# Performance work log

Measured on AMD Instinct MI355X. Metric: run time of the kernel, lower is better.

The kernel has to match this reference:

```python
import jax, jax.numpy as jnp
import numpy as np

N = 8
A_NUM = 5
ALPHA = [0.01, 0.25, 0.5, 0.9, 0.99]
EPS = 1e-10
BATCH = 262144


def _cayley(bias, n):
    # Build lower-triangular matrix exactly as torch code: row i+1 gets bias[i:2*i+1]
    b = bias.reshape(-1)
    L = jnp.zeros((n, n), dtype=bias.dtype)
    for i in range(n - 1):  # tiny fixed loop (n=8)
        L = L.at[i + 1, : i + 1].set(b[i : 2 * i + 1])
    Bm = L - L.T  # antisymmetric
    I = jnp.eye(n, dtype=bias.dtype)
    # MatrixExp = inv(I - Bm) @ (I + Bm)  (Cayley transform)
    return jnp.linalg.solve(I - Bm, I + Bm)


def _translate(A, bias, n):
    Q = _cayley(bias, n)
    # Q @ A @ Q^T, batched over leading dim
    return jnp.einsum('ij,bjk,lk->bil', Q, A, Q)


def _nus(M, W, eps):
    # weighted sum over the a_num axis with normalized squared weights
    w = W[:, 0] ** 2
    w = w / (w.sum() + eps)
    return jnp.einsum('a,banm->bnm', w, M)


def setup_inputs() -> dict:
    key = jax.random.key(0)
    ks = jax.random.split(key, 9)
    n2 = N * N
    return {
        'x': jax.random.normal(ks[0], (BATCH, n2), dtype=jnp.float32),
        'states': jax.random.normal(ks[1], (BATCH, A_NUM * n2), dtype=jnp.float32),
        'kernel_r': jax.random.uniform(ks[2], (A_NUM, 1), dtype=jnp.float32),
        'kernel_t': jax.random.uniform(ks[3], (1, 1), dtype=jnp.float32),
        'kernel_phi': jax.random.uniform(ks[4], (1, 1), dtype=jnp.float32),
        'kernel_s': jax.random.uniform(ks[5], (A_NUM, 1), dtype=jnp.float32),
        'bias_r': jax.random.uniform(ks[6], (N * (N - 1) // 2, 1), dtype=jnp.float32),
        'bias_t': jax.random.uniform(ks[7], (N * (N - 1) // 2, 1), dtype=jnp.float32),
        'bias_y': jax.random.uniform(ks[8], (N * (N - 1) // 2, 1), dtype=jnp.float32),
    }


def reference(x, states, kernel_r, kernel_t, kernel_phi, kernel_s, bias_r, bias_t, bias_y):
    n, a_num, eps = N, A_NUM, EPS
    Xt = x.reshape(-1, n, n)
    Mt_1 = states.reshape(-1, a_num, n, n)

    Yt = _nus(Mt_1, kernel_r, eps)              # [B,n,n]
    Rt = _translate(Yt, bias_r, n)

    t = kernel_t ** 2 / (kernel_t ** 2 + kernel_phi ** 2 + eps)  # (1,1) scalar gate
    Tt = (1.0 - t) * Xt + t * Rt                # FM
    Phit = _translate(Tt, bias_t, n)

    alpha = jnp.asarray(ALPHA, dtype=x.dtype)[None, :, None, None]
    Mt = (1.0 - alpha) * Mt_1 + alpha * Phit[:, None, :, :]      # [B,a,n,n]

    St = _nus(Mt, kernel_s, eps)
    Ot = _translate(St, bias_y, n)

    output = Ot.reshape(-1, n * n)
    out_state = Mt.reshape(-1, a_num * n * n)
    return output, out_state
```

## Files before the change

### kernel.cpp

```cpp
#include <hip/hip_runtime.h>

#define ANUM 5
#define EPS 1e-10f

__global__ void precompute_kernel(const float* __restrict__ kernel_r,
                                  const float* __restrict__ kernel_t,
                                  const float* __restrict__ kernel_phi,
                                  const float* __restrict__ kernel_s,
                                  const float* __restrict__ bias_r,
                                  const float* __restrict__ bias_t,
                                  const float* __restrict__ bias_y,
                                  float* __restrict__ ws) {
  __shared__ float sQ[3][64];
  const int tid = threadIdx.x;
  if (tid < 3) {
    const float* bias = (tid == 0) ? bias_r : (tid == 1) ? bias_t : bias_y;

    float Bm[8][8];
#pragma unroll
    for (int a = 0; a < 8; ++a)
#pragma unroll
      for (int b = 0; b < 8; ++b) Bm[a][b] = 0.f;
#pragma unroll
    for (int a = 0; a < 7; ++a) {
#pragma unroll 8
      for (int c = 0; c < 7; ++c) {
        if (c <= a) {
          float v = bias[a + c];
          Bm[a + 1][c] = v;
          Bm[c][a + 1] = -v;
        }
      }
    }
    float A[8][8], C[8][8];
#pragma unroll
    for (int a = 0; a < 8; ++a)
#pragma unroll
      for (int b = 0; b < 8; ++b) {
        float id = (a == b) ? 1.f : 0.f;
        A[a][b] = id - Bm[a][b];
        C[a][b] = id + Bm[a][b];
      }
#pragma unroll
    for (int p = 0; p < 8; ++p) {
      float inv = 1.f / A[p][p];
#pragma unroll
      for (int b = 0; b < 8; ++b) { A[p][b] *= inv; C[p][b] *= inv; }
#pragma unroll
      for (int r = 0; r < 8; ++r) {
        if (r == p) continue;
        float f = A[r][p];
#pragma unroll
        for (int b = 0; b < 8; ++b) { A[r][b] -= f * A[p][b]; C[r][b] -= f * C[p][b]; }
      }
    }
#pragma unroll
    for (int a = 0; a < 8; ++a)
#pragma unroll
      for (int b = 0; b < 8; ++b) sQ[tid][a * 8 + b] = C[a][b];
  } else if (tid == 3) {
    float sr = 0.f, ss = 0.f;
#pragma unroll
    for (int a = 0; a < ANUM; ++a) sr += kernel_r[a] * kernel_r[a];
#pragma unroll
    for (int a = 0; a < ANUM; ++a) ws[192 + a] = kernel_r[a] * kernel_r[a] / (sr + EPS);
#pragma unroll
    for (int a = 0; a < ANUM; ++a) ss += kernel_s[a] * kernel_s[a];
#pragma unroll
    for (int a = 0; a < ANUM; ++a) ws[197 + a] = kernel_s[a] * kernel_s[a] / (ss + EPS);
    float kt2 = kernel_t[0] * kernel_t[0];
    float kp2 = kernel_phi[0] * kernel_phi[0];
    ws[202] = kt2 / (kt2 + kp2 + EPS);
  }
  __syncthreads();
  const int i = tid >> 3, j = tid & 7;
  float acc = 0.f;
#pragma unroll
  for (int k = 0; k < 8; ++k) acc += sQ[1][i * 8 + k] * sQ[0][k * 8 + j];
  ws[tid]       = sQ[1][tid];
  ws[64 + tid]  = acc;
  ws[128 + tid] = sQ[2][tid];
}

__device__ __forceinline__ float dot8(float4 a0, float4 a1, float4 b0, float4 b1) {
  return a0.x * b0.x + a0.y * b0.y + a0.z * b0.z + a0.w * b0.w +
         a1.x * b1.x + a1.y * b1.y + a1.z * b1.z + a1.w * b1.w;
}

#define LGKM0() asm volatile("s_waitcnt lgkmcnt(0)" ::: "memory")

__launch_bounds__(256, 4)
__global__ void spdsru_kernel(const float* __restrict__ x,
                              const float* __restrict__ states,
                              const float* __restrict__ ws,
                              float* __restrict__ out,
                              float* __restrict__ out_state,
                              int B, int ITER, int W) {
  __shared__ __align__(16) float lds[4][4][64];
  const int tid = threadIdx.x;
  const int lane = tid & 63;
  const int wv = tid >> 6;
  const int i = lane >> 3, j = lane & 7;
  float* b0 = lds[wv][0];
  float* b1 = lds[wv][1];
  float* b2 = lds[wv][2];
  float* b3 = lds[wv][3];

  const float4 Qti0 = *(const float4*)(ws + 0 + i * 8);
  const float4 Qti1 = *(const float4*)(ws + 0 + i * 8 + 4);
  const float4 Qtj0 = *(const float4*)(ws + 0 + j * 8);
  const float4 Qtj1 = *(const float4*)(ws + 0 + j * 8 + 4);
  const float4 Q1i0 = *(const float4*)(ws + 64 + i * 8);
  const float4 Q1i1 = *(const float4*)(ws + 64 + i * 8 + 4);
  const float4 Q1j0 = *(const float4*)(ws + 64 + j * 8);
  const float4 Q1j1 = *(const float4*)(ws + 64 + j * 8 + 4);
  const float4 Qyi0 = *(const float4*)(ws + 128 + i * 8);
  const float4 Qyi1 = *(const float4*)(ws + 128 + i * 8 + 4);
  const float4 Qyj0 = *(const float4*)(ws + 128 + j * 8);
  const float4 Qyj1 = *(const float4*)(ws + 128 + j * 8 + 4);
  const float wr0 = ws[192], wr1 = ws[193], wr2 = ws[194], wr3 = ws[195], wr4 = ws[196];
  const float ks0 = ws[197], ks1 = ws[198], ks2 = ws[199], ks3 = ws[200], ks4 = ws[201];
  const float tg = ws[202];

  const int wave = (blockIdx.x * 256 + tid) >> 6;

  int b = wave;
  float X = 0.f, M0 = 0.f, M1 = 0.f, M2 = 0.f, M3 = 0.f, M4 = 0.f;
  if (b < B) {
    const float* S = states + (size_t)b * 320;
    X  = x[(size_t)b * 64 + lane];
    M0 = S[0 * 64 + lane];
    M1 = S[1 * 64 + lane];
    M2 = S[2 * 64 + lane];
    M3 = S[3 * 64 + lane];
    M4 = S[4 * 64 + lane];
  }

  for (int it = 0; it < ITER; ++it) {
    const int bn = b + W;
    float Xn = 0.f, N0 = 0.f, N1 = 0.f, N2 = 0.f, N3 = 0.f, N4 = 0.f;
    if (it + 1 < ITER && bn < B) {
      const float* Sn = states + (size_t)bn * 320;
      Xn = x[(size_t)bn * 64 + lane];
      N0 = Sn[0 * 64 + lane];
      N1 = Sn[1 * 64 + lane];
      N2 = Sn[2 * 64 + lane];
      N3 = Sn[3 * 64 + lane];
      N4 = Sn[4 * 64 + lane];
    }

    const float Yt = wr0 * M0 + wr1 * M1 + wr2 * M2 + wr3 * M3 + wr4 * M4;

    b0[lane] = X;
    b2[lane] = Yt;
    LGKM0();
    {
      float4 xr0 = *(const float4*)(b0 + i * 8);
      float4 xr1 = *(const float4*)(b0 + i * 8 + 4);
      float4 yr0 = *(const float4*)(b2 + i * 8);
      float4 yr1 = *(const float4*)(b2 + i * 8 + 4);
      float vx = dot8(xr0, xr1, Qtj0, Qtj1);
      float vy = dot8(yr0, yr1, Q1j0, Q1j1);
      b1[j * 8 + i] = vx;
      b3[j * 8 + i] = vy;
    }
    LGKM0();
    float XT, YT;
    {
      float4 xc0 = *(const float4*)(b1 + j * 8);
      float4 xc1 = *(const float4*)(b1 + j * 8 + 4);
      float4 yc0 = *(const float4*)(b3 + j * 8);
      float4 yc1 = *(const float4*)(b3 + j * 8 + 4);
      XT = dot8(xc0, xc1, Qti0, Qti1);
      YT = dot8(yc0, yc1, Q1i0, Q1i1);
    }
    const float Ph = (1.f - tg) * XT + tg * YT;

    M0 = (1.0f - 0.01f) * M0 + 0.01f * Ph;
    M1 = (1.0f - 0.25f) * M1 + 0.25f * Ph;
    M2 = (1.0f - 0.5f)  * M2 + 0.5f  * Ph;
    M3 = (1.0f - 0.9f)  * M3 + 0.9f  * Ph;
    M4 = (1.0f - 0.99f) * M4 + 0.99f * Ph;

    if (b < B) {
      float* SO = out_state + (size_t)b * 320;
      SO[0 * 64 + lane] = M0;
      SO[1 * 64 + lane] = M1;
      SO[2 * 64 + lane] = M2;
      SO[3 * 64 + lane] = M3;
      SO[4 * 64 + lane] = M4;
    }

    const float St = ks0 * M0 + ks1 * M1 + ks2 * M2 + ks3 * M3 + ks4 * M4;
    b0[lane] = St;
    LGKM0();
    {
      float4 r0 = *(const float4*)(b0 + i * 8);
      float4 r1 = *(const float4*)(b0 + i * 8 + 4);
      float v = dot8(r0, r1, Qyj0, Qyj1);
      b1[j * 8 + i] = v;
    }
    LGKM0();
    float Ot;
    {
      float4 c0 = *(const float4*)(b1 + j * 8);
      float4 c1 = *(const float4*)(b1 + j * 8 + 4);
      Ot = dot8(c0, c1, Qyi0, Qyi1);
    }
    if (b < B) out[(size_t)b * 64 + lane] = Ot;

    X = Xn; M0 = N0; M1 = N1; M2 = N2; M3 = N3; M4 = N4;
    b = bn;
  }
}

extern "C" void kernel_launch(void* const* d_in, const int* in_sizes, int n_in,
                              void* d_out, int out_size, void* d_ws, size_t ws_size,
                              hipStream_t stream) {
  const float* x          = (const float*)d_in[0];
  const float* states     = (const float*)d_in[1];
  const float* kernel_r   = (const float*)d_in[2];
  const float* kernel_t   = (const float*)d_in[3];
  const float* kernel_phi = (const float*)d_in[4];
  const float* kernel_s   = (const float*)d_in[5];
  const float* bias_r     = (const float*)d_in[6];
  const float* bias_t     = (const float*)d_in[7];
  const float* bias_y     = (const float*)d_in[8];
  float* ws = (float*)d_ws;
  float* out = (float*)d_out;

  const int B = in_sizes[0] / 64;
  float* out_state = out + (size_t)B * 64;

  precompute_kernel<<<1, 64, 0, stream>>>(kernel_r, kernel_t, kernel_phi, kernel_s,
                                          bias_r, bias_t, bias_y, ws);

  const int blocks = 2048;
  const int W = blocks * 4;
  const int ITER = (B + W - 1) / W;
  spdsru_kernel<<<blocks, 256, 0, stream>>>(x, states, ws, out, out_state, B, ITER, W);
}
```

Measured before the change: 665.3 us.

## Fold output translate into one LDS round via precomposed Cayley products

Expands St algebraically into a mix of the old states, X and Y. The output rotation is then computed in the same two LDS transpose rounds as the Phi path, using precomposed matrices Qy*Qt and Qy*Qt*Qr scaled by square-root gate factors. This removes the serial dependency on the state update and two extra LDS round trips per matrix. In exchange each lane does more dot products and holds more matrix registers. The launch bound drops its minimum occupancy hint, and sqrt-based scaling may shift rounding slightly.

```diff
diff --git a/kernel.cpp b/kernel.cpp
--- a/kernel.cpp
+++ b/kernel.cpp
@@ -11,7 +11,7 @@
                                   const float* __restrict__ bias_t,
                                   const float* __restrict__ bias_y,
                                   float* __restrict__ ws) {
-  __shared__ float sQ[3][64];
+  __shared__ float sQ[4][64];
   const int tid = threadIdx.x;
   if (tid < 3) {
     const float* bias = (tid == 0) ? bias_r : (tid == 1) ? bias_t : bias_y;
@@ -58,28 +58,48 @@
     for (int a = 0; a < 8; ++a)
 #pragma unroll
       for (int b = 0; b < 8; ++b) sQ[tid][a * 8 + b] = C[a][b];
-  } else if (tid == 3) {
-    float sr = 0.f, ss = 0.f;
-#pragma unroll
-    for (int a = 0; a < ANUM; ++a) sr += kernel_r[a] * kernel_r[a];
-#pragma unroll
-    for (int a = 0; a < ANUM; ++a) ws[192 + a] = kernel_r[a] * kernel_r[a] / (sr + EPS);
-#pragma unroll
-    for (int a = 0; a < ANUM; ++a) ss += kernel_s[a] * kernel_s[a];
-#pragma unroll
-    for (int a = 0; a < ANUM; ++a) ws[197 + a] = kernel_s[a] * kernel_s[a] / (ss + EPS);
-    float kt2 = kernel_t[0] * kernel_t[0];
-    float kp2 = kernel_phi[0] * kernel_phi[0];
-    ws[202] = kt2 / (kt2 + kp2 + EPS);
   }
   __syncthreads();
   const int i = tid >> 3, j = tid & 7;
-  float acc = 0.f;
-#pragma unroll
-  for (int k = 0; k < 8; ++k) acc += sQ[1][i * 8 + k] * sQ[0][k * 8 + j];
-  ws[tid]       = sQ[1][tid];
-  ws[64 + tid]  = acc;
-  ws[128 + tid] = sQ[2][tid];
+  float q1 = 0.f;
+#pragma unroll
+  for (int k = 0; k < 8; ++k) q1 += sQ[1][i * 8 + k] * sQ[0][k * 8 + j];
+  sQ[3][tid] = q1;
+  __syncthreads();
+  float q2 = 0.f, q3 = 0.f;
+#pragma unroll
+  for (int k = 0; k < 8; ++k) {
+    q2 += sQ[2][i * 8 + k] * sQ[1][k * 8 + j];
+    q3 += sQ[2][i * 8 + k] * sQ[3][k * 8 + j];
+  }
+  float sr = 0.f, ss = 0.f;
+#pragma unroll
+  for (int a = 0; a < ANUM; ++a) sr += kernel_r[a] * kernel_r[a];
+#pragma unroll
+  for (int a = 0; a < ANUM; ++a) ss += kernel_s[a] * kernel_s[a];
+  const float alpha[ANUM] = {0.01f, 0.25f, 0.5f, 0.9f, 0.99f};
+  float c = 0.f;
+#pragma unroll
+  for (int a = 0; a < ANUM; ++a)
+    c += (kernel_s[a] * kernel_s[a] / (ss + EPS)) * alpha[a];
+  float kt2 = kernel_t[0] * kernel_t[0];
+  float kp2 = kernel_phi[0] * kernel_phi[0];
+  float t = kt2 / (kt2 + kp2 + EPS);
+
+  const float s1 = sqrtf(1.f - t);
+  const float s2 = sqrtf(t);
+  const float s3 = sqrtf(c * (1.f - t));
+  const float s4 = sqrtf(c * t);
+
+  ws[tid]        = sQ[1][tid] * s1;
+  ws[64 + tid]   = sQ[3][tid] * s2;
+  ws[128 + tid]  = sQ[2][tid];
+  ws[192 + tid]  = q2 * s3;
+  ws[256 + tid]  = q3 * s4;
+  if (tid < ANUM) {
+    ws[320 + tid] = kernel_r[tid] * kernel_r[tid] / (sr + EPS);
+    ws[325 + tid] = (kernel_s[tid] * kernel_s[tid] / (ss + EPS)) * (1.f - alpha[tid]);
+  }
 }
 
 __device__ __forceinline__ float dot8(float4 a0, float4 a1, float4 b0, float4 b1) {
@@ -88,39 +108,41 @@
 }
 
 #define LGKM0() asm volatile("s_waitcnt lgkmcnt(0)" ::: "memory")
-
-__launch_bounds__(256, 4)
+#define UNI(nm, idx) \
+  const float nm = __int_as_float(__builtin_amdgcn_readfirstlane(__float_as_int(ws[idx])));
+
+__launch_bounds__(256)
 __global__ void spdsru_kernel(const float* __restrict__ x,
                               const float* __restrict__ states,
                               const float* __restrict__ ws,
                               float* __restrict__ out,
                               float* __restrict__ out_state,
                               int B, int ITER, int W) {
-  __shared__ __align__(16) float lds[4][4][64];
+  __shared__ __align__(16) float lds[4][5][64];
   const int tid = threadIdx.x;
   const int lane = tid & 63;
   const int wv = tid >> 6;
   const int i = lane >> 3, j = lane & 7;
-  float* b0 = lds[wv][0];
-  float* b1 = lds[wv][1];
-  float* b2 = lds[wv][2];
+  float* bX = lds[wv][0];
+  float* bY = lds[wv][1];
+  float* bS = lds[wv][2];
   float* b3 = lds[wv][3];
-
-  const float4 Qti0 = *(const float4*)(ws + 0 + i * 8);
-  const float4 Qti1 = *(const float4*)(ws + 0 + i * 8 + 4);
-  const float4 Qtj0 = *(const float4*)(ws + 0 + j * 8);
-  const float4 Qtj1 = *(const float4*)(ws + 0 + j * 8 + 4);
-  const float4 Q1i0 = *(const float4*)(ws + 64 + i * 8);
-  const float4 Q1i1 = *(const float4*)(ws + 64 + i * 8 + 4);
-  const float4 Q1j0 = *(const float4*)(ws + 64 + j * 8);
-  const float4 Q1j1 = *(const float4*)(ws + 64 + j * 8 + 4);
-  const float4 Qyi0 = *(const float4*)(ws + 128 + i * 8);
-  const float4 Qyi1 = *(const float4*)(ws + 128 + i * 8 + 4);
-  const float4 Qyj0 = *(const float4*)(ws + 128 + j * 8);
-  const float4 Qyj1 = *(const float4*)(ws + 128 + j * 8 + 4);
-  const float wr0 = ws[192], wr1 = ws[193], wr2 = ws[194], wr3 = ws[195], wr4 = ws[196];
-  const float ks0 = ws[197], ks1 = ws[198], ks2 = ws[199], ks3 = ws[200], ks4 = ws[201];
-  const float tg = ws[202];
+  float* b4 = lds[wv][4];
+
+#define LOADQ(nm, off)                                          \
+  const float4 nm##i0 = *(const float4*)(ws + off + i * 8);     \
+  const float4 nm##i1 = *(const float4*)(ws + off + i * 8 + 4); \
+  const float4 nm##j0 = *(const float4*)(ws + off + j * 8);     \
+  const float4 nm##j1 = *(const float4*)(ws + off + j * 8 + 4);
+  LOADQ(Qt, 0)
+  LOADQ(Q1, 64)
+  LOADQ(Qy, 128)
+  LOADQ(Q2, 192)
+  LOADQ(Q3, 256)
+#undef LOADQ
+
+  UNI(wr0, 320) UNI(wr1, 321) UNI(wr2, 322) UNI(wr3, 323) UNI(wr4, 324)
+  UNI(w20, 325) UNI(w21, 326) UNI(w22, 327) UNI(w23, 328) UNI(w24, 329)
 
   const int wave = (blockIdx.x * 256 + tid) >> 6;
 
@@ -150,32 +172,51 @@
     }
 
     const float Yt = wr0 * M0 + wr1 * M1 + wr2 * M2 + wr3 * M3 + wr4 * M4;
-
-    b0[lane] = X;
-    b2[lane] = Yt;
+    const float S0 = w20 * M0 + w21 * M1 + w22 * M2 + w23 * M3 + w24 * M4;
+
+    bX[lane] = X;
+    bY[lane] = Yt;
+    bS[lane] = S0;
     LGKM0();
     {
-      float4 xr0 = *(const float4*)(b0 + i * 8);
-      float4 xr1 = *(const float4*)(b0 + i * 8 + 4);
-      float4 yr0 = *(const float4*)(b2 + i * 8);
-      float4 yr1 = *(const float4*)(b2 + i * 8 + 4);
-      float vx = dot8(xr0, xr1, Qtj0, Qtj1);
-      float vy = dot8(yr0, yr1, Q1j0, Q1j1);
-      b1[j * 8 + i] = vx;
-      b3[j * 8 + i] = vy;
+      float4 xr0 = *(const float4*)(bX + i * 8);
+      float4 xr1 = *(const float4*)(bX + i * 8 + 4);
+      float4 yr0 = *(const float4*)(bY + i * 8);
+      float4 yr1 = *(const float4*)(bY + i * 8 + 4);
+      float4 sr0 = *(const float4*)(bS + i * 8);
+      float4 sr1 = *(const float4*)(bS + i * 8 + 4);
+      float vXT = dot8(xr0, xr1, Qtj0, Qtj1);
+      float vX2 = dot8(xr0, xr1, Q2j0, Q2j1);
+      float vY1 = dot8(yr0, yr1, Q1j0, Q1j1);
+      float vY3 = dot8(yr0, yr1, Q3j0, Q3j1);
+      float vSY = dot8(sr0, sr1, Qyj0, Qyj1);
+      const int tr = j * 8 + i;
+      bX[tr] = vXT;
+      bY[tr] = vY1;
+      bS[tr] = vSY;
+      b3[tr] = vX2;
+      b4[tr] = vY3;
     }
     LGKM0();
-    float XT, YT;
+    float XT, X2, Y1, Y3, SY;
     {
-      float4 xc0 = *(const float4*)(b1 + j * 8);
-      float4 xc1 = *(const float4*)(b1 + j * 8 + 4);
-      float4 yc0 = *(const float4*)(b3 + j * 8);
-      float4 yc1 = *(const float4*)(b3 + j * 8 + 4);
-      XT = dot8(xc0, xc1, Qti0, Qti1);
-      YT = dot8(yc0, yc1, Q1i0, Q1i1);
-    }
-    const float Ph = (1.f - tg) * XT + tg * YT;
-
+      float4 c0, c1;
+      c0 = *(const float4*)(bX + j * 8); c1 = *(const float4*)(bX + j * 8 + 4);
+      XT = dot8(c0, c1, Qti0, Qti1);
+      c0 = *(const float4*)(bY + j * 8); c1 = *(const float4*)(bY + j * 8 + 4);
+      Y1 = dot8(c0, c1, Q1i0, Q1i1);
+      c0 = *(const float4*)(bS + j * 8); c1 = *(const float4*)(bS + j * 8 + 4);
+      SY = dot8(c0, c1, Qyi0, Qyi1);
+      c0 = *(const float4*)(b3 + j * 8); c1 = *(const float4*)(b3 + j * 8 + 4);
+      X2 = dot8(c0, c1, Q2i0, Q2i1);
+      c0 = *(const float4*)(b4 + j * 8); c1 = *(const float4*)(b4 + j * 8 + 4);
+      Y3 = dot8(c0, c1, Q3i0, Q3i1);
+    }
+
+    const float Ot = SY + X2 + Y3;
+    if (b < B) out[(size_t)b * 64 + lane] = Ot;
+
+    const float Ph = XT + Y1;
     M0 = (1.0f - 0.01f) * M0 + 0.01f * Ph;
     M1 = (1.0f - 0.25f) * M1 + 0.25f * Ph;
     M2 = (1.0f - 0.5f)  * M2 + 0.5f  * Ph;
@@ -190,24 +231,6 @@
       SO[3 * 64 + lane] = M3;
       SO[4 * 64 + lane] = M4;
     }
-
-    const float St = ks0 * M0 + ks1 * M1 + ks2 * M2 + ks3 * M3 + ks4 * M4;
-    b0[lane] = St;
-    LGKM0();
-    {
-      float4 r0 = *(const float4*)(b0 + i * 8);
-      float4 r1 = *(const float4*)(b0 + i * 8 + 4);
-      float v = dot8(r0, r1, Qyj0, Qyj1);
-      b1[j * 8 + i] = v;
-    }
-    LGKM0();
-    float Ot;
-    {
-      float4 c0 = *(const float4*)(b1 + j * 8);
-      float4 c1 = *(const float4*)(b1 + j * 8 + 4);
-      Ot = dot8(c0, c1, Qyi0, Qyi1);
-    }
-    if (b < B) out[(size_t)b * 64 + lane] = Ot;
 
     X = Xn; M0 = N0; M1 = N1; M2 = N2; M3 = N3; M4 = N4;
     b = bn;
```

After: 670.6 us. About the same (+0.8%).
